# Optimization experiments

Hardware: AMD Instinct MI355X
Metric: run time of the kernel (lower is better)

## Reference

```python
import jax, jax.numpy as jnp
import numpy as np

K = 3          # kernel size
S = 1          # stride
P = 1          # padding
D = 1          # dilation
KK = K * K


def conv2d(x, w, b):
    # plain conv for the offset branch, NCHW/OIHW
    out = jax.lax.conv_general_dilated(
        x, w, window_strides=(S, S), padding=[(P, P), (P, P)],
        rhs_dilation=(D, D), dimension_numbers=('NCHW', 'OIHW', 'NCHW'))
    return out + b[None, :, None, None]


def deform_conv2d(x, offset, w, b):
    # torchvision-style deformable conv (groups=1, no modulation mask)
    B, C, H, W = x.shape
    Cout = w.shape[0]
    Ho, Wo = offset.shape[2], offset.shape[3]
    # offset channels are interleaved (dy, dx) per kernel tap
    off = offset.reshape(B, KK, 2, Ho, Wo)
    dy, dx = off[:, :, 0], off[:, :, 1]                      # [B,KK,Ho,Wo]

    ki, kj = jnp.meshgrid(jnp.arange(K), jnp.arange(K), indexing='ij')
    ki = ki.reshape(KK).astype(x.dtype)
    kj = kj.reshape(KK).astype(x.dtype)
    base_y = (jnp.arange(Ho) * S - P).astype(x.dtype)
    base_x = (jnp.arange(Wo) * S - P).astype(x.dtype)
    # absolute sampling coords per (b, tap, ho, wo)
    py = base_y[None, None, :, None] + (ki * D)[None, :, None, None] + dy
    px = base_x[None, None, None, :] + (kj * D)[None, :, None, None] + dx

    y0f = jnp.floor(py)
    x0f = jnp.floor(px)
    wy1 = py - y0f
    wx1 = px - x0f
    wy0 = 1.0 - wy1
    wx0 = 1.0 - wx1
    y0 = y0f.astype(jnp.int32)
    x0 = x0f.astype(jnp.int32)

    x_flat = x.reshape(B, C, H * W)

    def gather(yi, xi):
        # zero-padded gather at integer corner (yi, xi): [B,KK,Ho,Wo] -> [B,C,KK,Ho,Wo]
        valid = (yi >= 0) & (yi < H) & (xi >= 0) & (xi < W)
        idx = jnp.clip(yi, 0, H - 1) * W + jnp.clip(xi, 0, W - 1)
        v = jax.vmap(lambda xf, i: xf[:, i])(x_flat, idx.reshape(B, -1))
        v = v.reshape(B, C, KK, Ho, Wo)
        return v * valid[:, None].astype(x.dtype)

    v00 = gather(y0, x0)
    v01 = gather(y0, x0 + 1)
    v10 = gather(y0 + 1, x0)
    v11 = gather(y0 + 1, x0 + 1)

    sampled = ((wy0 * wx0)[:, None] * v00 + (wy0 * wx1)[:, None] * v01 +
               (wy1 * wx0)[:, None] * v10 + (wy1 * wx1)[:, None] * v11)
    # implicit GEMM over (Cin, kernel taps)
    out = jnp.einsum('bckhw,ock->bohw', sampled, w.reshape(Cout, C, KK))
    return out + b[None, :, None, None]


def setup_inputs() -> dict:
    key = jax.random.key(0)
    k1, k2, k3 = jax.random.split(key, 3)
    B, Cin, Cout, H, W = 32, 64, 64, 64, 64
    x = jax.random.normal(k1, (B, Cin, H, W), dtype=jnp.float32)
    # small but nonzero offset weights so bilinear sampling is exercised
    w_offset = jax.random.normal(k2, (2 * KK, Cin, K, K), dtype=jnp.float32) * 0.01
    b_offset = jnp.zeros((2 * KK,), dtype=jnp.float32)
    fan_in = Cin * KK
    w_conv = jax.random.normal(k3, (Cout, Cin, K, K), dtype=jnp.float32) * (1.0 / np.sqrt(fan_in))
    b_conv = jnp.zeros((Cout,), dtype=jnp.float32)
    return {'x': x, 'w_offset': w_offset, 'b_offset': b_offset,
            'w_conv': w_conv, 'b_conv': b_conv}


def reference(x, w_offset, b_offset, w_conv, b_conv):
    offset = conv2d(x, w_offset, b_offset)       # [B, 2*K*K, Ho, Wo]
    return deform_conv2d(x, offset, w_conv, b_conv)
```

## Files before the change

### kernel.cpp

```cpp
#include <hip/hip_runtime.h>
#include <hip/hip_bf16.h>

#define CIN  64
#define COUT 64
#define HH   64
#define WW   64
#define HW   4096
#define OFFC 18
#define KK2  9
#define II   576
#define NP   16
#define SMPW (II + 8)
#define NKC  (II / 32)
#define IMGB (HW * CIN * 2)

typedef __attribute__((ext_vector_type(8))) short  short8;
typedef __attribute__((ext_vector_type(4))) float  f32x4;

__device__ __forceinline__ float u2f(unsigned int u) {
    union { unsigned int i; float f; } v; v.i = u; return v.f;
}
__device__ __forceinline__ short8 as_short8(uint4 u) {
    union { uint4 a; short8 b; } v; v.a = u; return v.b;
}

__global__ __launch_bounds__(256) void transpose_x(const float* __restrict__ x,
                                                   __hip_bfloat16* __restrict__ xT) {
    __shared__ float tile[64][65];
    const int bh = blockIdx.x;
    const int b = bh >> 6, h = bh & 63;
    {
        const int w = threadIdx.x & 63, cg = threadIdx.x >> 6;
        #pragma unroll
        for (int c = cg; c < 64; c += 4)
            tile[c][w] = x[((b * 64 + c) * 64 + h) * 64 + w];
    }
    __syncthreads();
    {
        const int c = threadIdx.x & 63, wg = threadIdx.x >> 6;
        #pragma unroll
        for (int w = wg; w < 64; w += 4)
            xT[((b * 64 + h) * 64 + w) * 64 + c] = __float2bfloat16(tile[c][w]);
    }
}

__global__ __launch_bounds__(256) void pack_weights(const float* __restrict__ wc,
                                                    const float* __restrict__ w,
                                                    __hip_bfloat16* __restrict__ wmp,
                                                    __hip_bfloat16* __restrict__ bop) {
    const int idx = blockIdx.x * 256 + threadIdx.x;
    if (idx < 4 * NKC * 64 * 8) {
        const int j    = idx & 7;
        const int lane = (idx >> 3) & 63;
        const int kc   = (idx >> 9) % NKC;
        const int nt   = idx / (NKC * 512);
        const int o  = nt * 16 + (lane & 15);
        const int ks = kc * 32 + (lane >> 4) * 8 + j;
        const int c  = ks & 63, kk = ks >> 6;
        wmp[idx] = __float2bfloat16(wc[(o * CIN + c) * KK2 + kk]);
    } else {
        const int i2 = idx - 4 * NKC * 64 * 8;
        const int j    = i2 & 7;
        const int lane = (i2 >> 3) & 63;
        const int kc   = (i2 >> 9) % NKC;
        const int nt   = i2 / (NKC * 512);
        const int ch = nt * 16 + (lane & 15);
        const int ks = kc * 32 + (lane >> 4) * 8 + j;
        const int c  = ks & 63, kk = ks >> 6;
        bop[i2] = (ch < OFFC) ? __float2bfloat16(w[(ch * CIN + c) * KK2 + kk])
                              : __float2bfloat16(0.f);
    }
}

__global__ __launch_bounds__(256, 2) void offset_meta(const __hip_bfloat16* __restrict__ xT,
                                                      const __hip_bfloat16* __restrict__ bop,
                                                      const float* __restrict__ boff,
                                                      uint4* __restrict__ gmeta) {
    __shared__ float offs[64][20];
    const int t = threadIdx.x;
    const int wave = t >> 6, lane = t & 63;
    const int bh = blockIdx.x;
    const int b = bh >> 6, ho = bh & 63;
    const char* xbB = (const char*)xT + (size_t)b * IMGB;
    const int wo0 = wave * 16;
    const int m = lane & 15, quad = lane >> 4;

    f32x4 acc0 = {0.f, 0.f, 0.f, 0.f};
    f32x4 acc1 = {0.f, 0.f, 0.f, 0.f};
    const short8* bp = (const short8*)bop;
    #pragma unroll
    for (int ki = 0; ki < 3; ++ki) {
        const int y  = ho - 1 + ki;
        const int yl = min(max(y, 0), 63);
        const bool yok = (unsigned)y < HH;
        uint4 av[6];
        #pragma unroll
        for (int kj = 0; kj < 3; ++kj) {
            const int col = wo0 + m + kj - 1;
            const int ccl = min(max(col, 0), WW - 1);
            const bool ok = yok & ((unsigned)col < WW);
            const char* base = xbB + (yl * 64 + ccl) * 128 + quad * 16;
            #pragma unroll
            for (int h = 0; h < 2; ++h) {
                uint4 v = *(const uint4*)(base + h * 64);
                if (!ok) { v.x = 0u; v.y = 0u; v.z = 0u; v.w = 0u; }
                av[kj * 2 + h] = v;
            }
        }
        #pragma unroll
        for (int kj = 0; kj < 3; ++kj) {
            #pragma unroll
            for (int h = 0; h < 2; ++h) {
                const int kc = 2 * (ki * 3 + kj) + h;
                const short8 a = as_short8(av[kj * 2 + h]);
                acc0 = __builtin_amdgcn_mfma_f32_16x16x32_bf16(a, bp[kc * 64 + lane], acc0, 0, 0, 0);
                acc1 = __builtin_amdgcn_mfma_f32_16x16x32_bf16(a, bp[(NKC + kc) * 64 + lane], acc1, 0, 0, 0);
            }
        }
    }
    {
        const int ch0 = lane & 15;
        const int ch1 = 16 + ch0;
        const float bias0 = boff[ch0];
        const float bias1 = (ch1 < OFFC) ? boff[ch1] : 0.f;
        #pragma unroll
        for (int r = 0; r < 4; ++r) {
            const int p = wo0 + quad * 4 + r;
            offs[p][ch0] = acc0[r] + bias0;
            if (ch1 < OFFC) offs[p][ch1] = acc1[r] + bias1;
        }
    }
    __syncthreads();

    for (int e = t; e < 64 * KK2; e += 256) {
        const int p = e / KK2, kk = e - p * KK2;
        const int wo = p;
        const float dy = offs[p][2 * kk];
        const float dx = offs[p][2 * kk + 1];
        const int ki = kk / 3, kj = kk - ki * 3;
        const float py = (float)(ho - 1 + ki) + dy;
        const float px = (float)(wo - 1 + kj) + dx;
        const float y0f = floorf(py), x0f = floorf(px);
        const int y0 = (int)y0f, x0 = (int)x0f;
        const float wy1 = py - y0f, wx1 = px - x0f;
        const float wy0 = 1.f - wy1, wx0 = 1.f - wx1;
        const int yb = min(max(y0, 0), HH - 2);
        const int zb = min(max(x0, 0), WW - 2);
        const float vy0 = ((unsigned)y0 < HH) ? wy0 : 0.f;
        const float vy1 = ((unsigned)(y0 + 1) < HH) ? wy1 : 0.f;
        const float vx0 = ((unsigned)x0 < WW) ? wx0 : 0.f;
        const float vx1 = ((unsigned)(x0 + 1) < WW) ? wx1 : 0.f;
        const float t0 = (y0 == yb ? vy0 : 0.f) + (y0 + 1 == yb ? vy1 : 0.f);
        const float t1 = (y0 == yb + 1 ? vy0 : 0.f) + (y0 + 1 == yb + 1 ? vy1 : 0.f);
        const float u0 = (x0 == zb ? vx0 : 0.f) + (x0 + 1 == zb ? vx1 : 0.f);
        const float u1 = (x0 == zb + 1 ? vx0 : 0.f) + (x0 + 1 == zb + 1 ? vx1 : 0.f);
        union { unsigned int u; _Float16 h[2]; } c0, c1;
        c0.h[0] = (_Float16)(t0 * u0); c0.h[1] = (_Float16)(t1 * u0);
        c1.h[0] = (_Float16)(t0 * u1); c1.h[1] = (_Float16)(t1 * u1);
        uint4 mt;
        mt.x = (unsigned int)((yb * 64 + zb) * 128);
        mt.y = c0.u; mt.z = c1.u; mt.w = 0u;
        gmeta[(size_t)bh * 576 + e] = mt;
    }
}

__global__ __launch_bounds__(256, 6) void deform_main(const __hip_bfloat16* __restrict__ xT,
                                                      const __hip_bfloat16* __restrict__ wmp,
                                                      const float* __restrict__ bconv,
                                                      const uint4* __restrict__ gmeta,
                                                      float* __restrict__ out) {
    __shared__ __hip_bfloat16 smp[NP][SMPW];
    __shared__ uint4 metal[NP * KK2];

    const int t = threadIdx.x;
    const int wave = t >> 6, lane = t & 63;
    const int sp0g = blockIdx.x * NP;
    const int b = sp0g >> 12, sp0 = sp0g & 4095;
    const char* xbB = (const char*)xT + (size_t)b * IMGB;

    if (t < NP * KK2) metal[t] = gmeta[(size_t)blockIdx.x * (NP * KK2) + t];
    __syncthreads();

    {
        const int li = lane & 31;
        const int h  = lane >> 5;
        const char* xli = xbB + li * 4;
        for (int q = 0; q < 4; ++q) {
            const int p = wave * 4 + q;
            uint4 mtj[5];
            #pragma unroll
            for (int j = 0; j < 5; ++j) {
                const int kk = min(2 * j + h, 8);
                mtj[j] = metal[p * KK2 + kk];
            }
            unsigned int rg[5][4];
            #pragma unroll
            for (int j = 0; j < 5; ++j) {
                const char* base = xli + (int)mtj[j].x;
                rg[j][0] = *(const unsigned int*)(base);
                rg[j][1] = *(const unsigned int*)(base + 128);
                rg[j][2] = *(const unsigned int*)(base + 8192);
                rg[j][3] = *(const unsigned int*)(base + 8320);
            }
            #pragma unroll
            for (int j = 0; j < 5; ++j) {
                union { unsigned int u; _Float16 f[2]; } c0, c1;
                c0.u = mtj[j].y; c1.u = mtj[j].z;
                const float w00 = (float)c0.f[0], w10 = (float)c0.f[1];
                const float w01 = (float)c1.f[0], w11 = (float)c1.f[1];
                const float a0l = u2f(rg[j][0] << 16), a0h = u2f(rg[j][0] & 0xffff0000u);
                const float a1l = u2f(rg[j][1] << 16), a1h = u2f(rg[j][1] & 0xffff0000u);
                const float b0l = u2f(rg[j][2] << 16), b0h = u2f(rg[j][2] & 0xffff0000u);
                const float b1l = u2f(rg[j][3] << 16), b1h = u2f(rg[j][3] & 0xffff0000u);
                const float vl = w00 * a0l + w01 * a1l + w10 * b0l + w11 * b1l;
                const float vh = w00 * a0h + w01 * a1h + w10 * b0h + w11 * b1h;
                const int kk = min(2 * j + h, 8);
                __hip_bfloat162 pk;
                pk.x = __float2bfloat16(vl);
                pk.y = __float2bfloat16(vh);
                *(__hip_bfloat162*)((char*)&smp[p][0] + kk * 128 + li * 4) = pk;
            }
        }
    }
    __syncthreads();

    f32x4 acc = {0.f, 0.f, 0.f, 0.f};
    {
        const char* abase = (const char*)&smp[lane & 15][0] + (lane >> 4) * 16;
        const short8* wp = (const short8*)wmp + wave * NKC * 64 + lane;
        #pragma unroll
        for (int kc = 0; kc < NKC; ++kc) {
            const short8 a  = *(const short8*)(abase + kc * 64);
            const short8 bw = wp[kc * 64];
            acc = __builtin_amdgcn_mfma_f32_16x16x32_bf16(a, bw, acc, 0, 0, 0);
        }
    }
    __syncthreads();

    {
        float* outb = (float*)&smp[0][0];
        const int o = wave * 16 + (lane & 15);
        const float bias = bconv[o];
        const int pr = (lane >> 4) * 4;
        #pragma unroll
        for (int r = 0; r < 4; ++r)
            outb[o * 17 + pr + r] = acc[r] + bias;
    }
    __syncthreads();
    {
        const float* outb = (const float*)&smp[0][0];
        const int oo = t >> 2, pxb = (t & 3) * 4;
        const float* lb = outb + oo * 17 + pxb;
        float4 v;
        v.x = lb[0]; v.y = lb[1]; v.z = lb[2]; v.w = lb[3];
        *(float4*)(out + ((size_t)(b * COUT + oo)) * HW + sp0 + pxb) = v;
    }
}

extern "C" void kernel_launch(void* const* d_in, const int* in_sizes, int n_in,
                              void* d_out, int out_size, void* d_ws, size_t ws_size,
                              hipStream_t stream) {
    const float* x      = (const float*)d_in[0];
    const float* w_off  = (const float*)d_in[1];
    const float* b_off  = (const float*)d_in[2];
    const float* w_conv = (const float*)d_in[3];
    const float* b_conv = (const float*)d_in[4];
    float* out = (float*)d_out;

    __hip_bfloat16* xT  = (__hip_bfloat16*)d_ws;
    __hip_bfloat16* wmp = xT + (size_t)32 * HW * CIN;
    __hip_bfloat16* bop = wmp + 4 * NKC * 64 * 8;
    uint4* gmeta = (uint4*)((char*)d_ws + 16887808);

    hipLaunchKernelGGL(transpose_x,  dim3(32 * HH), dim3(256), 0, stream, x, xT);
    hipLaunchKernelGGL(pack_weights, dim3(55296 / 256), dim3(256), 0, stream, w_conv, w_off, wmp, bop);
    hipLaunchKernelGGL(offset_meta,  dim3(32 * HH), dim3(256), 0, stream, xT, bop, b_off, gmeta);
    hipLaunchKernelGGL(deform_main,  dim3(32 * HW / NP), dim3(256), 0, stream,
                       xT, wmp, b_conv, gmeta, out);
}
```

Measured before the change: 170.1 us.

## Fuse offset conv and metadata into main deform kernel; merge prep kernels

Merges the x transpose and weight packing into one prep kernel and vectorizes the transpose loads and stores. It folds the offset-conv MFMA and bilinear metadata computation into the main deform kernel per 16-pixel block, splitting the 9 taps across the 4 waves with a shared-memory reduction. This removes the global gmeta round trip and two kernel launches. The offset conv is now computed per 16-pixel tile with less parallelism per wave, and two extra block barriers are added.

```diff
diff --git a/kernel.cpp b/kernel.cpp
--- a/kernel.cpp
+++ b/kernel.cpp
@@ -23,120 +23,142 @@
 __device__ __forceinline__ short8 as_short8(uint4 u) {
     union { uint4 a; short8 b; } v; v.a = u; return v.b;
 }
-
-__global__ __launch_bounds__(256) void transpose_x(const float* __restrict__ x,
-                                                   __hip_bfloat16* __restrict__ xT) {
-    __shared__ float tile[64][65];
-    const int bh = blockIdx.x;
-    const int b = bh >> 6, h = bh & 63;
-    {
-        const int w = threadIdx.x & 63, cg = threadIdx.x >> 6;
-        #pragma unroll
-        for (int c = cg; c < 64; c += 4)
-            tile[c][w] = x[((b * 64 + c) * 64 + h) * 64 + w];
-    }
-    __syncthreads();
-    {
-        const int c = threadIdx.x & 63, wg = threadIdx.x >> 6;
-        #pragma unroll
-        for (int w = wg; w < 64; w += 4)
-            xT[((b * 64 + h) * 64 + w) * 64 + c] = __float2bfloat16(tile[c][w]);
-    }
-}
-
-__global__ __launch_bounds__(256) void pack_weights(const float* __restrict__ wc,
-                                                    const float* __restrict__ w,
-                                                    __hip_bfloat16* __restrict__ wmp,
-                                                    __hip_bfloat16* __restrict__ bop) {
-    const int idx = blockIdx.x * 256 + threadIdx.x;
-    if (idx < 4 * NKC * 64 * 8) {
-        const int j    = idx & 7;
-        const int lane = (idx >> 3) & 63;
-        const int kc   = (idx >> 9) % NKC;
-        const int nt   = idx / (NKC * 512);
-        const int o  = nt * 16 + (lane & 15);
-        const int ks = kc * 32 + (lane >> 4) * 8 + j;
-        const int c  = ks & 63, kk = ks >> 6;
-        wmp[idx] = __float2bfloat16(wc[(o * CIN + c) * KK2 + kk]);
+__device__ __forceinline__ unsigned short f2bf_bits(float f) {
+    union { __hip_bfloat16 b; unsigned short s; } cv;
+    cv.b = __float2bfloat16(f);
+    return cv.s;
+}
+
+__global__ __launch_bounds__(256) void prep(const float* __restrict__ x,
+                                            const float* __restrict__ wc,
+                                            const float* __restrict__ w,
+                                            __hip_bfloat16* __restrict__ xT,
+                                            __hip_bfloat16* __restrict__ wmp,
+                                            __hip_bfloat16* __restrict__ bop) {
+    const int t = threadIdx.x;
+    if (blockIdx.x < 2048) {
+        __shared__ float tile[64][68];
+        const int b = blockIdx.x >> 6, h = blockIdx.x & 63;
+        {
+            const int w4 = t & 15, cg = t >> 4;
+            #pragma unroll
+            for (int i = 0; i < 4; ++i) {
+                const int c = cg + i * 16;
+                const float4 v = *(const float4*)&x[((b * 64 + c) * 64 + h) * 64 + w4 * 4];
+                *(float4*)&tile[c][w4 * 4] = v;
+            }
+        }
+        __syncthreads();
+        {
+            const int ww = t & 63, c0 = (t >> 6) * 16;
+            unsigned int pk[8];
+            #pragma unroll
+            for (int ci = 0; ci < 8; ++ci) {
+                const unsigned int lo = f2bf_bits(tile[c0 + 2 * ci][ww]);
+                const unsigned int hi = f2bf_bits(tile[c0 + 2 * ci + 1][ww]);
+                pk[ci] = lo | (hi << 16);
+            }
+            char* dst = (char*)xT + (size_t)(((b * 64 + h) * 64 + ww) * 64 + c0) * 2;
+            uint4 v0, v1;
+            v0.x = pk[0]; v0.y = pk[1]; v0.z = pk[2]; v0.w = pk[3];
+            v1.x = pk[4]; v1.y = pk[5]; v1.z = pk[6]; v1.w = pk[7];
+            *(uint4*)dst = v0;
+            *(uint4*)(dst + 16) = v1;
+        }
     } else {
-        const int i2 = idx - 4 * NKC * 64 * 8;
-        const int j    = i2 & 7;
-        const int lane = (i2 >> 3) & 63;
-        const int kc   = (i2 >> 9) % NKC;
-        const int nt   = i2 / (NKC * 512);
-        const int ch = nt * 16 + (lane & 15);
-        const int ks = kc * 32 + (lane >> 4) * 8 + j;
-        const int c  = ks & 63, kk = ks >> 6;
-        bop[i2] = (ch < OFFC) ? __float2bfloat16(w[(ch * CIN + c) * KK2 + kk])
-                              : __float2bfloat16(0.f);
-    }
-}
-
-__global__ __launch_bounds__(256, 2) void offset_meta(const __hip_bfloat16* __restrict__ xT,
-                                                      const __hip_bfloat16* __restrict__ bop,
-                                                      const float* __restrict__ boff,
-                                                      uint4* __restrict__ gmeta) {
-    __shared__ float offs[64][20];
+        const int idx = (blockIdx.x - 2048) * 256 + t;
+        if (idx < 4 * NKC * 64 * 8) {
+            const int j    = idx & 7;
+            const int lane = (idx >> 3) & 63;
+            const int kc   = (idx >> 9) % NKC;
+            const int nt   = idx / (NKC * 512);
+            const int o  = nt * 16 + (lane & 15);
+            const int ks = kc * 32 + (lane >> 4) * 8 + j;
+            const int c  = ks & 63, kk = ks >> 6;
+            wmp[idx] = __float2bfloat16(wc[(o * CIN + c) * KK2 + kk]);
+        } else {
+            const int i2 = idx - 4 * NKC * 64 * 8;
+            const int j    = i2 & 7;
+            const int lane = (i2 >> 3) & 63;
+            const int kc   = (i2 >> 9) % NKC;
+            const int nt   = i2 / (NKC * 512);
+            const int ch = nt * 16 + (lane & 15);
+            const int ks = kc * 32 + (lane >> 4) * 8 + j;
+            const int c  = ks & 63, kk = ks >> 6;
+            bop[i2] = (ch < OFFC) ? __float2bfloat16(w[(ch * CIN + c) * KK2 + kk])
+                                  : __float2bfloat16(0.f);
+        }
+    }
+}
+
+__global__ __launch_bounds__(256, 6) void deform_fused(const __hip_bfloat16* __restrict__ xT,
+                                                       const __hip_bfloat16* __restrict__ bop,
+                                                       const __hip_bfloat16* __restrict__ wmp,
+                                                       const float* __restrict__ boff,
+                                                       const float* __restrict__ bconv,
+                                                       float* __restrict__ out) {
+    __shared__ __hip_bfloat16 smp[NP][SMPW];
+    __shared__ uint4 metal[NP * KK2];
+
     const int t = threadIdx.x;
     const int wave = t >> 6, lane = t & 63;
-    const int bh = blockIdx.x;
-    const int b = bh >> 6, ho = bh & 63;
+    const int sp0g = blockIdx.x * NP;
+    const int b = sp0g >> 12, sp0 = sp0g & 4095;
+    const int ho = sp0 >> 6, wo0 = sp0 & 63;
     const char* xbB = (const char*)xT + (size_t)b * IMGB;
-    const int wo0 = wave * 16;
-    const int m = lane & 15, quad = lane >> 4;
 
     f32x4 acc0 = {0.f, 0.f, 0.f, 0.f};
     f32x4 acc1 = {0.f, 0.f, 0.f, 0.f};
-    const short8* bp = (const short8*)bop;
-    #pragma unroll
-    for (int ki = 0; ki < 3; ++ki) {
-        const int y  = ho - 1 + ki;
-        const int yl = min(max(y, 0), 63);
-        const bool yok = (unsigned)y < HH;
-        uint4 av[6];
-        #pragma unroll
-        for (int kj = 0; kj < 3; ++kj) {
-            const int col = wo0 + m + kj - 1;
-            const int ccl = min(max(col, 0), WW - 1);
-            const bool ok = yok & ((unsigned)col < WW);
-            const char* base = xbB + (yl * 64 + ccl) * 128 + quad * 16;
-            #pragma unroll
-            for (int h = 0; h < 2; ++h) {
-                uint4 v = *(const uint4*)(base + h * 64);
-                if (!ok) { v.x = 0u; v.y = 0u; v.z = 0u; v.w = 0u; }
-                av[kj * 2 + h] = v;
-            }
-        }
-        #pragma unroll
-        for (int kj = 0; kj < 3; ++kj) {
-            #pragma unroll
-            for (int h = 0; h < 2; ++h) {
-                const int kc = 2 * (ki * 3 + kj) + h;
-                const short8 a = as_short8(av[kj * 2 + h]);
-                acc0 = __builtin_amdgcn_mfma_f32_16x16x32_bf16(a, bp[kc * 64 + lane], acc0, 0, 0, 0);
-                acc1 = __builtin_amdgcn_mfma_f32_16x16x32_bf16(a, bp[(NKC + kc) * 64 + lane], acc1, 0, 0, 0);
-            }
-        }
-    }
-    {
-        const int ch0 = lane & 15;
-        const int ch1 = 16 + ch0;
-        const float bias0 = boff[ch0];
-        const float bias1 = (ch1 < OFFC) ? boff[ch1] : 0.f;
+    {
+        const int m = lane & 15, quad = lane >> 4;
+        const short8* bp = (const short8*)bop;
+        for (int kk = wave; kk < KK2; kk += 4) {
+            const int ki = kk / 3, kj = kk - ki * 3;
+            const int y = ho - 1 + ki;
+            if ((unsigned)y < HH) {
+                const int col = wo0 + m + kj - 1;
+                const int ccl = min(max(col, 0), WW - 1);
+                const bool ok = (unsigned)col < WW;
+                const char* base = xbB + (y * 64 + ccl) * 128 + quad * 16;
+                uint4 v0 = *(const uint4*)(base);
+                uint4 v1 = *(const uint4*)(base + 64);
+                if (!ok) { v0.x = v0.y = v0.z = v0.w = 0u; v1.x = v1.y = v1.z = v1.w = 0u; }
+                const int kc0 = 2 * kk, kc1 = 2 * kk + 1;
+                acc0 = __builtin_amdgcn_mfma_f32_16x16x32_bf16(as_short8(v0), bp[kc0 * 64 + lane], acc0, 0, 0, 0);
+                acc1 = __builtin_amdgcn_mfma_f32_16x16x32_bf16(as_short8(v0), bp[(NKC + kc0) * 64 + lane], acc1, 0, 0, 0);
+                acc0 = __builtin_amdgcn_mfma_f32_16x16x32_bf16(as_short8(v1), bp[kc1 * 64 + lane], acc0, 0, 0, 0);
+                acc1 = __builtin_amdgcn_mfma_f32_16x16x32_bf16(as_short8(v1), bp[(NKC + kc1) * 64 + lane], acc1, 0, 0, 0);
+            }
+        }
+        float* pacc = (float*)&smp[0][0];
+        const int n = lane & 15;
         #pragma unroll
         for (int r = 0; r < 4; ++r) {
-            const int p = wo0 + quad * 4 + r;
-            offs[p][ch0] = acc0[r] + bias0;
-            if (ch1 < OFFC) offs[p][ch1] = acc1[r] + bias1;
-        }
-    }
-    __syncthreads();
-
-    for (int e = t; e < 64 * KK2; e += 256) {
-        const int p = e / KK2, kk = e - p * KK2;
-        const int wo = p;
-        const float dy = offs[p][2 * kk];
-        const float dx = offs[p][2 * kk + 1];
+            const int p = quad * 4 + r;
+            pacc[(wave * 16 + p) * 20 + n] = acc0[r];
+            if (n < 2) pacc[(wave * 16 + p) * 20 + 16 + n] = acc1[r];
+        }
+    }
+    __syncthreads();
+
+    {
+        float* pacc = (float*)&smp[0][0];
+        float* offs = pacc + 4 * 16 * 20;
+        for (int e = t; e < NP * OFFC; e += 256) {
+            const int p = e / OFFC, ch = e - p * OFFC;
+            offs[p * 20 + ch] = boff[ch]
+                + pacc[p * 20 + ch] + pacc[(16 + p) * 20 + ch]
+                + pacc[(32 + p) * 20 + ch] + pacc[(48 + p) * 20 + ch];
+        }
+    }
+    __syncthreads();
+
+    if (t < NP * KK2) {
+        const float* offs = (const float*)&smp[0][0] + 4 * 16 * 20;
+        const int p = t / KK2, kk = t - p * KK2;
+        const int wo = wo0 + p;
+        const float dy = offs[p * 20 + 2 * kk];
+        const float dx = offs[p * 20 + 2 * kk + 1];
         const int ki = kk / 3, kj = kk - ki * 3;
         const float py = (float)(ho - 1 + ki) + dy;
         const float px = (float)(wo - 1 + kj) + dx;
@@ -160,25 +182,8 @@
         uint4 mt;
         mt.x = (unsigned int)((yb * 64 + zb) * 128);
         mt.y = c0.u; mt.z = c1.u; mt.w = 0u;
-        gmeta[(size_t)bh * 576 + e] = mt;
-    }
-}
-
-__global__ __launch_bounds__(256, 6) void deform_main(const __hip_bfloat16* __restrict__ xT,
-                                                      const __hip_bfloat16* __restrict__ wmp,
-                                                      const float* __restrict__ bconv,
-                                                      const uint4* __restrict__ gmeta,
-                                                      float* __restrict__ out) {
-    __shared__ __hip_bfloat16 smp[NP][SMPW];
-    __shared__ uint4 metal[NP * KK2];
-
-    const int t = threadIdx.x;
-    const int wave = t >> 6, lane = t & 63;
-    const int sp0g = blockIdx.x * NP;
-    const int b = sp0g >> 12, sp0 = sp0g & 4095;
-    const char* xbB = (const char*)xT + (size_t)b * IMGB;
-
-    if (t < NP * KK2) metal[t] = gmeta[(size_t)blockIdx.x * (NP * KK2) + t];
+        metal[t] = mt;
+    }
     __syncthreads();
 
     {
@@ -270,11 +275,9 @@
     __hip_bfloat16* xT  = (__hip_bfloat16*)d_ws;
     __hip_bfloat16* wmp = xT + (size_t)32 * HW * CIN;
     __hip_bfloat16* bop = wmp + 4 * NKC * 64 * 8;
-    uint4* gmeta = (uint4*)((char*)d_ws + 16887808);
-
-    hipLaunchKernelGGL(transpose_x,  dim3(32 * HH), dim3(256), 0, stream, x, xT);
-    hipLaunchKernelGGL(pack_weights, dim3(55296 / 256), dim3(256), 0, stream, w_conv, w_off, wmp, bop);
-    hipLaunchKernelGGL(offset_meta,  dim3(32 * HH), dim3(256), 0, stream, xT, bop, b_off, gmeta);
-    hipLaunchKernelGGL(deform_main,  dim3(32 * HW / NP), dim3(256), 0, stream,
-                       xT, wmp, b_conv, gmeta, out);
-}
+
+    hipLaunchKernelGGL(prep, dim3(2048 + 216), dim3(256), 0, stream,
+                       x, w_conv, w_off, xT, wmp, bop);
+    hipLaunchKernelGGL(deform_fused, dim3(32 * HW / NP), dim3(256), 0, stream,
+                       xT, bop, wmp, b_off, b_conv, out);
+}
```

Result: faster. 159.4 us (-6.3%).
